# Kernel optimization log

Measured on AMD Instinct MI355X. Metric: run time of the kernel, lower is better.

## Reference

```python
import jax, jax.numpy as jnp
import numpy as np

B, C, H, W = 32, 512, 32, 32
K = 1024  # num_embeddings


def setup_inputs() -> dict:
    key = jax.random.key(0)
    k1, k2 = jax.random.split(key)
    z = jax.random.normal(k1, (B, C, H, W), dtype=jnp.float32)
    embedding = jax.random.normal(k2, (K, C), dtype=jnp.float32)
    return {"z": z, "embedding": embedding}


def reference(z, embedding):
    # NCHW -> NHWC, flatten to [N, C]
    zt = jnp.transpose(z, (0, 2, 3, 1))            # [B, H, W, C]
    z_flat = zt.reshape(-1, zt.shape[-1])          # [N, C]
    # squared-euclidean distances: ||z||^2 - 2 z.e^T + ||e||^2
    dist = (jnp.sum(z_flat ** 2, axis=1, keepdims=True)
            - 2.0 * z_flat @ embedding.T
            + jnp.sum(embedding ** 2, axis=1))     # [N, K]
    indices = jnp.argmin(dist, axis=1)             # [N]
    quantized = embedding[indices].reshape(zt.shape)  # [B, H, W, C]
    quantized = jnp.transpose(quantized, (0, 3, 1, 2))  # [B, C, H, W]
    return quantized, indices.reshape(z.shape[0], -1)
```

## Files before the change

### kernel.cpp

```cpp
#include <hip/hip_runtime.h>
#include <hip/hip_bf16.h>

#define CDIM 512
#define KDIM 1024
#define HW   1024
#define NPOS 32768
#define BM   128
#define BN   128
#define BK   64
#define NKS  (CDIM / BK)
#define NNB  (KDIM / BN)
#define TILE_USHORT (8 * 128 * 8)

typedef float  f32x16 __attribute__((ext_vector_type(16)));
typedef float  f4     __attribute__((ext_vector_type(4)));
typedef short  bf16x8 __attribute__((ext_vector_type(8)));
typedef unsigned int u32x4 __attribute__((ext_vector_type(4)));

static __device__ __forceinline__ unsigned short f2bf(float f) {
    __hip_bfloat16 h = __float2bfloat16(f);
    union { __hip_bfloat16 h; unsigned short u; } cv; cv.h = h; return cv.u;
}
static __device__ __forceinline__ float bf2f(unsigned short u) {
    union { unsigned short u; __hip_bfloat16 h; } cv; cv.u = u; return __bfloat162float(cv.h);
}

__global__ __launch_bounds__(64) void prep_e(const float* __restrict__ e,
                                             unsigned short* __restrict__ Bt_hi,
                                             unsigned short* __restrict__ Bt_lo,
                                             float* __restrict__ enorm) {
    const int k  = blockIdx.x;
    const int t  = threadIdx.x;
    const int nb = k >> 7, row = k & 127;
    const int ks = t >> 3, slot = t & 7;

    const f4* src = (const f4*)(e + (size_t)k * CDIM + ks * 64 + slot * 8);
    const f4 a = src[0], b = src[1];
    float v[8] = {a.x, a.y, a.z, a.w, b.x, b.y, b.z, b.w};

    unsigned int hw_[4], lw_[4];
    float ss = 0.0f;
    #pragma unroll
    for (int d = 0; d < 4; ++d) {
        const float v0 = v[2 * d], v1 = v[2 * d + 1];
        const unsigned short h0 = f2bf(v0), h1 = f2bf(v1);
        hw_[d] = (unsigned int)h0 | ((unsigned int)h1 << 16);
        lw_[d] = (unsigned int)f2bf(v0 - bf2f(h0)) |
                 ((unsigned int)f2bf(v1 - bf2f(h1)) << 16);
        ss += v0 * v0 + v1 * v1;
    }
    const size_t off = ((((size_t)nb * 8 + ks) * 8 + slot) * 128 + row) * 8;
    *(u32x4*)(Bt_hi + off) = u32x4{hw_[0], hw_[1], hw_[2], hw_[3]};
    *(u32x4*)(Bt_lo + off) = u32x4{lw_[0], lw_[1], lw_[2], lw_[3]};

    #pragma unroll
    for (int o = 32; o > 0; o >>= 1) ss += __shfl_down(ss, o, 64);
    if (t == 0) enorm[k] = ss;
}

__global__ __launch_bounds__(256) void vq_gemm(const float* __restrict__ z,
                                               const unsigned short* __restrict__ Bt_hi,
                                               const unsigned short* __restrict__ Bt_lo,
                                               const float* __restrict__ enorm,
                                               float2* __restrict__ part) {
    __shared__ unsigned short Ah[8][128][8], Al[8][128][8];
    __shared__ unsigned short Bh[8][128][8], Bl[8][128][8];
    __shared__ float lval[2][128];
    __shared__ int   lidx[2][128];

    const int bid = blockIdx.x;
    const int x = bid & 7, jj = bid >> 3;
    const int m  = x * 32 + (jj >> 3);
    const int nb = jj & 7;

    const int n0  = m * BM;
    const int b   = n0 >> 10;
    const int hw0 = n0 & 1023;

    const int t   = threadIdx.x;
    const int wid = t >> 6, l = t & 63;
    const int wr  = wid >> 1, wc = wid & 1;

    f32x16 acc[2][2];
    #pragma unroll
    for (int i = 0; i < 2; ++i)
        #pragma unroll
        for (int j = 0; j < 2; ++j) acc[i][j] = (f32x16)0.0f;

    const float* zbase = z + (size_t)b * CDIM * HW + hw0;
    const int sp = t & 127;
    const int sh = t >> 7;

    float v[32];
    u32x4 bhv[4], blv[4];

    {
        const float* zc = zbase + (size_t)(sh * 32) * HW + sp;
        #pragma unroll
        for (int i = 0; i < 32; ++i) v[i] = zc[(size_t)i * HW];
        const u32x4* bsh = (const u32x4*)(Bt_hi + (size_t)nb * 8 * TILE_USHORT);
        const u32x4* bsl = (const u32x4*)(Bt_lo + (size_t)nb * 8 * TILE_USHORT);
        #pragma unroll
        for (int q = 0; q < 4; ++q) { bhv[q] = bsh[q * 256 + t]; blv[q] = bsl[q * 256 + t]; }
    }

    #pragma unroll
    for (int ks = 0; ks < NKS; ++ks) {
        __syncthreads();

        #pragma unroll
        for (int o = 0; o < 4; ++o) {
            unsigned int hw_[4], lw_[4];
            #pragma unroll
            for (int d = 0; d < 4; ++d) {
                const float a0 = v[o * 8 + 2 * d], a1 = v[o * 8 + 2 * d + 1];
                const unsigned short h0 = f2bf(a0), h1 = f2bf(a1);
                hw_[d] = (unsigned int)h0 | ((unsigned int)h1 << 16);
                lw_[d] = (unsigned int)f2bf(a0 - bf2f(h0)) |
                         ((unsigned int)f2bf(a1 - bf2f(h1)) << 16);
            }
            *(u32x4*)&Ah[sh * 4 + o][sp][0] = u32x4{hw_[0], hw_[1], hw_[2], hw_[3]};
            *(u32x4*)&Al[sh * 4 + o][sp][0] = u32x4{lw_[0], lw_[1], lw_[2], lw_[3]};
        }
        unsigned short* bhp = &Bh[0][0][0];
        unsigned short* blp = &Bl[0][0][0];
        #pragma unroll
        for (int q = 0; q < 4; ++q) {
            *(u32x4*)(bhp + (size_t)(q * 256 + t) * 8) = bhv[q];
            *(u32x4*)(blp + (size_t)(q * 256 + t) * 8) = blv[q];
        }
        __syncthreads();

        if (ks + 1 < NKS) {
            const float* zc = zbase + (size_t)((ks + 1) * 64 + sh * 32) * HW + sp;
            #pragma unroll
            for (int i = 0; i < 32; ++i) v[i] = zc[(size_t)i * HW];
            const u32x4* bsh = (const u32x4*)(Bt_hi + ((size_t)nb * 8 + ks + 1) * TILE_USHORT);
            const u32x4* bsl = (const u32x4*)(Bt_lo + ((size_t)nb * 8 + ks + 1) * TILE_USHORT);
            #pragma unroll
            for (int q = 0; q < 4; ++q) { bhv[q] = bsh[q * 256 + t]; blv[q] = bsl[q * 256 + t]; }
        }

        #pragma unroll
        for (int ksub = 0; ksub < 4; ++ksub) {
            const int so = 2 * ksub + (l >> 5);
            const int cr = wr * 64 + (l & 31);
            const int pr = wc * 64 + (l & 31);
            const bf16x8 ch0 = *(const bf16x8*)&Bh[so][cr][0];
            const bf16x8 ch1 = *(const bf16x8*)&Bh[so][cr + 32][0];
            const bf16x8 cl0 = *(const bf16x8*)&Bl[so][cr][0];
            const bf16x8 cl1 = *(const bf16x8*)&Bl[so][cr + 32][0];
            const bf16x8 ph0 = *(const bf16x8*)&Ah[so][pr][0];
            const bf16x8 ph1 = *(const bf16x8*)&Ah[so][pr + 32][0];
            const bf16x8 pl0 = *(const bf16x8*)&Al[so][pr][0];
            const bf16x8 pl1 = *(const bf16x8*)&Al[so][pr + 32][0];
            acc[0][0] = __builtin_amdgcn_mfma_f32_32x32x16_bf16(ch0, ph0, acc[0][0], 0, 0, 0);
            acc[0][1] = __builtin_amdgcn_mfma_f32_32x32x16_bf16(ch0, ph1, acc[0][1], 0, 0, 0);
            acc[1][0] = __builtin_amdgcn_mfma_f32_32x32x16_bf16(ch1, ph0, acc[1][0], 0, 0, 0);
            acc[1][1] = __builtin_amdgcn_mfma_f32_32x32x16_bf16(ch1, ph1, acc[1][1], 0, 0, 0);
            acc[0][0] = __builtin_amdgcn_mfma_f32_32x32x16_bf16(ch0, pl0, acc[0][0], 0, 0, 0);
            acc[0][1] = __builtin_amdgcn_mfma_f32_32x32x16_bf16(ch0, pl1, acc[0][1], 0, 0, 0);
            acc[1][0] = __builtin_amdgcn_mfma_f32_32x32x16_bf16(ch1, pl0, acc[1][0], 0, 0, 0);
            acc[1][1] = __builtin_amdgcn_mfma_f32_32x32x16_bf16(ch1, pl1, acc[1][1], 0, 0, 0);
            acc[0][0] = __builtin_amdgcn_mfma_f32_32x32x16_bf16(cl0, ph0, acc[0][0], 0, 0, 0);
            acc[0][1] = __builtin_amdgcn_mfma_f32_32x32x16_bf16(cl0, ph1, acc[0][1], 0, 0, 0);
            acc[1][0] = __builtin_amdgcn_mfma_f32_32x32x16_bf16(cl1, ph0, acc[1][0], 0, 0, 0);
            acc[1][1] = __builtin_amdgcn_mfma_f32_32x32x16_bf16(cl1, ph1, acc[1][1], 0, 0, 0);
        }
    }

    const float* en = enorm + nb * 128 + wr * 64;
    #pragma unroll
    for (int pj = 0; pj < 2; ++pj) {
        float bv = 1e30f; int bi = 1 << 20;
        #pragma unroll
        for (int ci = 0; ci < 2; ++ci) {
            #pragma unroll
            for (int r = 0; r < 16; ++r) {
                const int code = ci * 32 + (r & 3) + 8 * (r >> 2) + 4 * (l >> 5);
                const float val = en[code] - 2.0f * acc[ci][pj][r];
                if (val < bv || (val == bv && code < bi)) { bv = val; bi = code; }
            }
        }
        const float ov = __shfl_xor(bv, 32, 64);
        const int   oi = __shfl_xor(bi, 32, 64);
        if (ov < bv || (ov == bv && oi < bi)) { bv = ov; bi = oi; }
        if (l < 32) { lval[wr][wc * 64 + pj * 32 + l] = bv; lidx[wr][wc * 64 + pj * 32 + l] = bi; }
    }
    __syncthreads();

    if (t < 128) {
        const float v0 = lval[0][t]; const int i0 = lidx[0][t];
        const float v1 = lval[1][t]; const int i1 = lidx[1][t] + 64;
        float bv = v0; int bi = i0;
        if (v1 < bv || (v1 == bv && i1 < bi)) { bv = v1; bi = i1; }
        part[(size_t)(n0 + t) * 8 + nb] = make_float2(bv, (float)(nb * 128 + bi));
    }
}

__global__ __launch_bounds__(256) void vq_reduce(const float2* __restrict__ part,
                                                 const float* __restrict__ e,
                                                 float* __restrict__ out_q,
                                                 float* __restrict__ out_i) {
    __shared__ int bidx[128];
    const int t  = threadIdx.x;
    const int p0 = blockIdx.x * 128;

    if (t < 128) {
        const int n = p0 + t;
        const float2* pr = part + (size_t)n * 8;
        float bv = pr[0].x; int bi = (int)pr[0].y;
        #pragma unroll
        for (int nb = 1; nb < 8; ++nb) {
            const float2 c = pr[nb];
            const int ci = (int)c.y;
            if (c.x < bv || (c.x == bv && ci < bi)) { bv = c.x; bi = ci; }
        }
        bidx[t] = bi;
        out_i[n] = (float)bi;
    }
    __syncthreads();

    const int pq = t & 31;
    const int cs = t >> 5;
    const int n  = p0 + pq * 4;
    const int b  = n >> 10, hwp = n & 1023;

    const int r0 = bidx[pq * 4 + 0], r1 = bidx[pq * 4 + 1];
    const int r2 = bidx[pq * 4 + 2], r3 = bidx[pq * 4 + 3];
    const f4* e0 = (const f4*)(e + (size_t)r0 * CDIM) + cs * 16;
    const f4* e1 = (const f4*)(e + (size_t)r1 * CDIM) + cs * 16;
    const f4* e2 = (const f4*)(e + (size_t)r2 * CDIM) + cs * 16;
    const f4* e3 = (const f4*)(e + (size_t)r3 * CDIM) + cs * 16;
    float* oq = out_q + (size_t)b * CDIM * HW + hwp;

    #pragma unroll 4
    for (int q = 0; q < 16; ++q) {
        const f4 a = e0[q], bb = e1[q], c = e2[q], d = e3[q];
        const int cbase = cs * 64 + q * 4;
        *(f4*)(oq + (size_t)(cbase + 0) * HW) = f4{a.x, bb.x, c.x, d.x};
        *(f4*)(oq + (size_t)(cbase + 1) * HW) = f4{a.y, bb.y, c.y, d.y};
        *(f4*)(oq + (size_t)(cbase + 2) * HW) = f4{a.z, bb.z, c.z, d.z};
        *(f4*)(oq + (size_t)(cbase + 3) * HW) = f4{a.w, bb.w, c.w, d.w};
    }
}

extern "C" void kernel_launch(void* const* d_in, const int* in_sizes, int n_in,
                              void* d_out, int out_size, void* d_ws, size_t ws_size,
                              hipStream_t stream) {
    const float* z = (const float*)d_in[0];
    const float* e = (const float*)d_in[1];

    float* out_q = (float*)d_out;
    float* out_i = out_q + (out_size - NPOS);

    unsigned short* Bt_hi = (unsigned short*)d_ws;
    unsigned short* Bt_lo = Bt_hi + (size_t)KDIM * CDIM;
    float*  enorm = (float*)(Bt_lo + (size_t)KDIM * CDIM);
    float2* part  = (float2*)((char*)d_ws + 2 * 1048576 + 4096);

    prep_e<<<KDIM, 64, 0, stream>>>(e, Bt_hi, Bt_lo, enorm);
    vq_gemm<<<(NPOS / BM) * NNB, 256, 0, stream>>>(z, Bt_hi, Bt_lo, enorm, part);
    vq_reduce<<<NPOS / 128, 256, 0, stream>>>(part, e, out_q, out_i);
}
```

Baseline: 239.3 us.

## Pre-split z into bf16 tiles and stream GEMM operands via async LDS loads

```diff
diff --git a/kernel.cpp b/kernel.cpp
--- a/kernel.cpp
+++ b/kernel.cpp
@@ -7,10 +7,10 @@
 #define NPOS 32768
 #define BM   128
 #define BN   128
-#define BK   64
-#define NKS  (CDIM / BK)
-#define NNB  (KDIM / BN)
-#define TILE_USHORT (8 * 128 * 8)
+#define BK   32
+#define NKS  16
+#define NNB  8
+#define PAY  8192
 
 typedef float  f32x16 __attribute__((ext_vector_type(16)));
 typedef float  f4     __attribute__((ext_vector_type(4)));
@@ -25,18 +25,24 @@
     union { unsigned short u; __hip_bfloat16 h; } cv; cv.u = u; return __bfloat162float(cv.h);
 }
 
+static __device__ __forceinline__ void gld16(const unsigned short* g, unsigned short* l) {
+    __builtin_amdgcn_global_load_lds(
+        (const __attribute__((address_space(1))) void*)g,
+        (__attribute__((address_space(3))) void*)l,
+        16, 0, 0);
+}
+
 __global__ __launch_bounds__(64) void prep_e(const float* __restrict__ e,
-                                             unsigned short* __restrict__ Bt_hi,
-                                             unsigned short* __restrict__ Bt_lo,
+                                             unsigned short* __restrict__ Bt,
                                              float* __restrict__ enorm) {
     const int k  = blockIdx.x;
     const int t  = threadIdx.x;
     const int nb = k >> 7, row = k & 127;
-    const int ks = t >> 3, slot = t & 7;
-
-    const f4* src = (const f4*)(e + (size_t)k * CDIM + ks * 64 + slot * 8);
+    const int ks = t >> 2, slot = t & 3;
+
+    const f4* src = (const f4*)(e + (size_t)k * CDIM + t * 8);
     const f4 a = src[0], b = src[1];
-    float v[8] = {a.x, a.y, a.z, a.w, b.x, b.y, b.z, b.w};
+    const float v[8] = {a.x, a.y, a.z, a.w, b.x, b.y, b.z, b.w};
 
     unsigned int hw_[4], lw_[4];
     float ss = 0.0f;
@@ -49,111 +55,114 @@
                  ((unsigned int)f2bf(v1 - bf2f(h1)) << 16);
         ss += v0 * v0 + v1 * v1;
     }
-    const size_t off = ((((size_t)nb * 8 + ks) * 8 + slot) * 128 + row) * 8;
-    *(u32x4*)(Bt_hi + off) = u32x4{hw_[0], hw_[1], hw_[2], hw_[3]};
-    *(u32x4*)(Bt_lo + off) = u32x4{lw_[0], lw_[1], lw_[2], lw_[3]};
+    const size_t base = (size_t)(nb * 16 + ks) * PAY + slot * 1024 + row * 8;
+    *(u32x4*)(Bt + base)        = u32x4{hw_[0], hw_[1], hw_[2], hw_[3]};
+    *(u32x4*)(Bt + base + 4096) = u32x4{lw_[0], lw_[1], lw_[2], lw_[3]};
 
     #pragma unroll
     for (int o = 32; o > 0; o >>= 1) ss += __shfl_down(ss, o, 64);
     if (t == 0) enorm[k] = ss;
 }
 
-__global__ __launch_bounds__(256) void vq_gemm(const float* __restrict__ z,
-                                               const unsigned short* __restrict__ Bt_hi,
-                                               const unsigned short* __restrict__ Bt_lo,
-                                               const float* __restrict__ enorm,
-                                               float2* __restrict__ part) {
-    __shared__ unsigned short Ah[8][128][8], Al[8][128][8];
-    __shared__ unsigned short Bh[8][128][8], Bl[8][128][8];
-    __shared__ float lval[2][128];
-    __shared__ int   lidx[2][128];
-
-    const int bid = blockIdx.x;
-    const int x = bid & 7, jj = bid >> 3;
-    const int m  = x * 32 + (jj >> 3);
-    const int nb = jj & 7;
-
-    const int n0  = m * BM;
-    const int b   = n0 >> 10;
-    const int hw0 = n0 & 1023;
-
-    const int t   = threadIdx.x;
-    const int wid = t >> 6, l = t & 63;
-    const int wr  = wid >> 1, wc = wid & 1;
-
-    f32x16 acc[2][2];
-    #pragma unroll
-    for (int i = 0; i < 2; ++i)
-        #pragma unroll
-        for (int j = 0; j < 2; ++j) acc[i][j] = (f32x16)0.0f;
-
-    const float* zbase = z + (size_t)b * CDIM * HW + hw0;
+__global__ __launch_bounds__(256) void prep_z(const float* __restrict__ z,
+                                              unsigned short* __restrict__ Az) {
+    const int m  = blockIdx.x;
+    const int t  = threadIdx.x;
+    const int b  = m >> 3;
+    const int hw0 = (m & 7) * 128;
     const int sp = t & 127;
     const int sh = t >> 7;
 
-    float v[32];
-    u32x4 bhv[4], blv[4];
-
-    {
-        const float* zc = zbase + (size_t)(sh * 32) * HW + sp;
-        #pragma unroll
-        for (int i = 0; i < 32; ++i) v[i] = zc[(size_t)i * HW];
-        const u32x4* bsh = (const u32x4*)(Bt_hi + (size_t)nb * 8 * TILE_USHORT);
-        const u32x4* bsl = (const u32x4*)(Bt_lo + (size_t)nb * 8 * TILE_USHORT);
-        #pragma unroll
-        for (int q = 0; q < 4; ++q) { bhv[q] = bsh[q * 256 + t]; blv[q] = bsl[q * 256 + t]; }
-    }
-
-    #pragma unroll
-    for (int ks = 0; ks < NKS; ++ks) {
-        __syncthreads();
-
-        #pragma unroll
-        for (int o = 0; o < 4; ++o) {
+    const float* zbase = z + (size_t)b * CDIM * HW + hw0 + sp;
+
+    #pragma unroll
+    for (int it = 0; it < 8; ++it) {
+        const int cbase = it * 64 + sh * 32;
+        float v[32];
+        #pragma unroll
+        for (int i = 0; i < 32; ++i) v[i] = zbase[(size_t)(cbase + i) * HW];
+
+        const int ks = it * 2 + sh;
+        const size_t tbase = (size_t)(m * 16 + ks) * PAY + sp * 8;
+        #pragma unroll
+        for (int slot = 0; slot < 4; ++slot) {
             unsigned int hw_[4], lw_[4];
             #pragma unroll
             for (int d = 0; d < 4; ++d) {
-                const float a0 = v[o * 8 + 2 * d], a1 = v[o * 8 + 2 * d + 1];
+                const float a0 = v[slot * 8 + 2 * d], a1 = v[slot * 8 + 2 * d + 1];
                 const unsigned short h0 = f2bf(a0), h1 = f2bf(a1);
                 hw_[d] = (unsigned int)h0 | ((unsigned int)h1 << 16);
                 lw_[d] = (unsigned int)f2bf(a0 - bf2f(h0)) |
                          ((unsigned int)f2bf(a1 - bf2f(h1)) << 16);
             }
-            *(u32x4*)&Ah[sh * 4 + o][sp][0] = u32x4{hw_[0], hw_[1], hw_[2], hw_[3]};
-            *(u32x4*)&Al[sh * 4 + o][sp][0] = u32x4{lw_[0], lw_[1], lw_[2], lw_[3]};
-        }
-        unsigned short* bhp = &Bh[0][0][0];
-        unsigned short* blp = &Bl[0][0][0];
-        #pragma unroll
-        for (int q = 0; q < 4; ++q) {
-            *(u32x4*)(bhp + (size_t)(q * 256 + t) * 8) = bhv[q];
-            *(u32x4*)(blp + (size_t)(q * 256 + t) * 8) = blv[q];
-        }
-        __syncthreads();
-
+            *(u32x4*)(Az + tbase + slot * 1024)        = u32x4{hw_[0], hw_[1], hw_[2], hw_[3]};
+            *(u32x4*)(Az + tbase + slot * 1024 + 4096) = u32x4{lw_[0], lw_[1], lw_[2], lw_[3]};
+        }
+    }
+}
+
+__global__ __launch_bounds__(256) void vq_gemm(const unsigned short* __restrict__ Az,
+                                               const unsigned short* __restrict__ Bt,
+                                               const float* __restrict__ enorm,
+                                               float2* __restrict__ part) {
+    __shared__ unsigned short lds[2][16384];
+    __shared__ float lval[2][128];
+    __shared__ int   lidx[2][128];
+
+    const int bid = blockIdx.x;
+    const int x = bid & 7, jj = bid >> 3;
+    const int m  = x * 32 + (jj >> 3);
+    const int nb = jj & 7;
+    const int n0 = m * BM;
+
+    const int t   = threadIdx.x;
+    const int wid = t >> 6, l = t & 63;
+    const int wr  = wid >> 1, wc = wid & 1;
+
+    const unsigned short* asrc = Az + (size_t)m  * NKS * PAY;
+    const unsigned short* bsrc = Bt + (size_t)nb * NKS * PAY;
+
+    f32x16 acc[2][2];
+    #pragma unroll
+    for (int i = 0; i < 2; ++i)
+        #pragma unroll
+        for (int j = 0; j < 2; ++j) acc[i][j] = (f32x16)0.0f;
+
+    #pragma unroll
+    for (int i = 0; i < 4; ++i) {
+        gld16(asrc + (size_t)(i * 256 + t) * 8, &lds[0][(i * 256 + t) * 8]);
+        gld16(bsrc + (size_t)(i * 256 + t) * 8, &lds[0][8192 + (i * 256 + t) * 8]);
+    }
+    __syncthreads();
+
+    const int pr = wc * 64 + (l & 31);
+    const int cr = wr * 64 + (l & 31);
+    const int lsel = l >> 5;
+
+    #pragma unroll
+    for (int ks = 0; ks < NKS; ++ks) {
+        const int cb = ks & 1;
         if (ks + 1 < NKS) {
-            const float* zc = zbase + (size_t)((ks + 1) * 64 + sh * 32) * HW + sp;
+            const unsigned short* an = asrc + (size_t)(ks + 1) * PAY;
+            const unsigned short* bn = bsrc + (size_t)(ks + 1) * PAY;
             #pragma unroll
-            for (int i = 0; i < 32; ++i) v[i] = zc[(size_t)i * HW];
-            const u32x4* bsh = (const u32x4*)(Bt_hi + ((size_t)nb * 8 + ks + 1) * TILE_USHORT);
-            const u32x4* bsl = (const u32x4*)(Bt_lo + ((size_t)nb * 8 + ks + 1) * TILE_USHORT);
-            #pragma unroll
-            for (int q = 0; q < 4; ++q) { bhv[q] = bsh[q * 256 + t]; blv[q] = bsl[q * 256 + t]; }
-        }
-
-        #pragma unroll
-        for (int ksub = 0; ksub < 4; ++ksub) {
-            const int so = 2 * ksub + (l >> 5);
-            const int cr = wr * 64 + (l & 31);
-            const int pr = wc * 64 + (l & 31);
-            const bf16x8 ch0 = *(const bf16x8*)&Bh[so][cr][0];
-            const bf16x8 ch1 = *(const bf16x8*)&Bh[so][cr + 32][0];
-            const bf16x8 cl0 = *(const bf16x8*)&Bl[so][cr][0];
-            const bf16x8 cl1 = *(const bf16x8*)&Bl[so][cr + 32][0];
-            const bf16x8 ph0 = *(const bf16x8*)&Ah[so][pr][0];
-            const bf16x8 ph1 = *(const bf16x8*)&Ah[so][pr + 32][0];
-            const bf16x8 pl0 = *(const bf16x8*)&Al[so][pr][0];
-            const bf16x8 pl1 = *(const bf16x8*)&Al[so][pr + 32][0];
+            for (int i = 0; i < 4; ++i) {
+                gld16(an + (size_t)(i * 256 + t) * 8, &lds[cb ^ 1][(i * 256 + t) * 8]);
+                gld16(bn + (size_t)(i * 256 + t) * 8, &lds[cb ^ 1][8192 + (i * 256 + t) * 8]);
+            }
+        }
+        __builtin_amdgcn_s_setprio(1);
+        #pragma unroll
+        for (int ksub = 0; ksub < 2; ++ksub) {
+            const int so = ksub * 2 + lsel;
+            const bf16x8 ch0 = *(const bf16x8*)&lds[cb][ 8192 + (so * 128 + cr) * 8];
+            const bf16x8 ch1 = *(const bf16x8*)&lds[cb][ 8192 + (so * 128 + cr + 32) * 8];
+            const bf16x8 cl0 = *(const bf16x8*)&lds[cb][12288 + (so * 128 + cr) * 8];
+            const bf16x8 cl1 = *(const bf16x8*)&lds[cb][12288 + (so * 128 + cr + 32) * 8];
+            const bf16x8 ph0 = *(const bf16x8*)&lds[cb][        (so * 128 + pr) * 8];
+            const bf16x8 ph1 = *(const bf16x8*)&lds[cb][        (so * 128 + pr + 32) * 8];
+            const bf16x8 pl0 = *(const bf16x8*)&lds[cb][ 4096 + (so * 128 + pr) * 8];
+            const bf16x8 pl1 = *(const bf16x8*)&lds[cb][ 4096 + (so * 128 + pr + 32) * 8];
             acc[0][0] = __builtin_amdgcn_mfma_f32_32x32x16_bf16(ch0, ph0, acc[0][0], 0, 0, 0);
             acc[0][1] = __builtin_amdgcn_mfma_f32_32x32x16_bf16(ch0, ph1, acc[0][1], 0, 0, 0);
             acc[1][0] = __builtin_amdgcn_mfma_f32_32x32x16_bf16(ch1, ph0, acc[1][0], 0, 0, 0);
@@ -167,6 +176,8 @@
             acc[1][0] = __builtin_amdgcn_mfma_f32_32x32x16_bf16(cl1, ph0, acc[1][0], 0, 0, 0);
             acc[1][1] = __builtin_amdgcn_mfma_f32_32x32x16_bf16(cl1, ph1, acc[1][1], 0, 0, 0);
         }
+        __builtin_amdgcn_s_setprio(0);
+        __syncthreads();
     }
 
     const float* en = enorm + nb * 128 + wr * 64;
@@ -177,7 +188,7 @@
         for (int ci = 0; ci < 2; ++ci) {
             #pragma unroll
             for (int r = 0; r < 16; ++r) {
-                const int code = ci * 32 + (r & 3) + 8 * (r >> 2) + 4 * (l >> 5);
+                const int code = ci * 32 + (r & 3) + 8 * (r >> 2) + 4 * lsel;
                 const float val = en[code] - 2.0f * acc[ci][pj][r];
                 if (val < bv || (val == bv && code < bi)) { bv = val; bi = code; }
             }
@@ -254,12 +265,14 @@
     float* out_q = (float*)d_out;
     float* out_i = out_q + (out_size - NPOS);
 
-    unsigned short* Bt_hi = (unsigned short*)d_ws;
-    unsigned short* Bt_lo = Bt_hi + (size_t)KDIM * CDIM;
-    float*  enorm = (float*)(Bt_lo + (size_t)KDIM * CDIM);
+    unsigned short* Az = (unsigned short*)d_out;
+
+    unsigned short* Bt = (unsigned short*)d_ws;
+    float*  enorm = (float*)((char*)d_ws + 2 * 1048576);
     float2* part  = (float2*)((char*)d_ws + 2 * 1048576 + 4096);
 
-    prep_e<<<KDIM, 64, 0, stream>>>(e, Bt_hi, Bt_lo, enorm);
-    vq_gemm<<<(NPOS / BM) * NNB, 256, 0, stream>>>(z, Bt_hi, Bt_lo, enorm, part);
+    prep_e<<<KDIM, 64, 0, stream>>>(e, Bt, enorm);
+    prep_z<<<256, 256, 0, stream>>>(z, Az);
+    vq_gemm<<<(NPOS / BM) * NNB, 256, 0, stream>>>(Az, Bt, enorm, part);
     vq_reduce<<<NPOS / 128, 256, 0, stream>>>(part, e, out_q, out_i);
 }
```

Result: no change. 235.3 us (-1.7%).
